# Performance work log

Measured on AMD Instinct MI355X. Metric: run time of the kernel, lower is better.

Reference implementation:

```python
import jax, jax.numpy as jnp
import numpy as np

LN_EPS = 1e-12


def layer_norm(x, g, b):
    mu = jnp.mean(x, axis=-1, keepdims=True)
    var = jnp.mean(jnp.square(x - mu), axis=-1, keepdims=True)
    return (x - mu) * jax.lax.rsqrt(var + LN_EPS) * g + b


def setup_inputs() -> dict:
    key = jax.random.key(0)
    ks = jax.random.split(key, 12)
    B, L, H, P, V = 8, 512, 768, 200, 30522
    src_scores = jax.random.normal(ks[0], (B, L, L), jnp.float32)
    seq_hidden = jax.random.normal(ks[1], (B, L, H), jnp.float32)
    seq_mask = jax.random.randint(ks[2], (B, L), 0, 2).astype(jnp.float32)
    pos_emb = jax.random.normal(ks[3], (512, P), jnp.float32) * 0.02
    Wp = jax.random.normal(ks[4], (H, P), jnp.float32) * 0.02
    bp = jnp.zeros((H,), jnp.float32)
    Wt = jax.random.normal(ks[5], (H, H), jnp.float32) * 0.02
    bt = jnp.zeros((H,), jnp.float32)
    ln_g = jnp.ones((H,), jnp.float32)
    ln_b = jnp.zeros((H,), jnp.float32)
    Wd = jax.random.normal(ks[6], (V, H), jnp.float32) * 0.02
    dec_bias = jnp.zeros((V,), jnp.float32)
    return dict(src_scores=src_scores, seq_hidden=seq_hidden, seq_mask=seq_mask,
                pos_emb=pos_emb, Wp=Wp, bp=bp, Wt=Wt, bt=bt,
                ln_g=ln_g, ln_b=ln_b, Wd=Wd, dec_bias=dec_bias)


def reference(src_scores, seq_hidden, seq_mask, pos_emb, Wp, bp, Wt, bt, ln_g, ln_b, Wd, dec_bias):
    L = src_scores.shape[1]
    # position embeddings for first L positions, projected to hidden size: [L, H]
    pos_h = pos_emb[:L] @ Wp.T + bp
    # pos_scores[b, l, s] = pos_h[l] . seq_hidden[b, s]
    pos_scores = jnp.einsum('lh,bsh->bls', pos_h, seq_hidden)
    scores = pos_scores + src_scores + seq_mask[:, None, :] * -10000.0
    alpha = jax.nn.softmax(scores, axis=-1)                 # [B, L, L]
    seq_sum = jnp.einsum('bls,bsh->blh', alpha, seq_hidden)  # [B, L, H]
    # BertPredictionHeadTransform: dense -> gelu (exact) -> LayerNorm
    h = layer_norm(jax.nn.gelu(seq_sum @ Wt.T + bt, approximate=False), ln_g, ln_b)
    target_scores = h @ Wd.T + dec_bias                      # [B, L, V]
    return target_scores
```

## Files before the change

kernel.cpp:

```cpp
#include <hip/hip_runtime.h>

using f32x4  = __attribute__((ext_vector_type(4))) float;
using short8 = __attribute__((ext_vector_type(8))) short;
using short4v= __attribute__((ext_vector_type(4))) short;
typedef __attribute__((ext_vector_type(8))) __bf16 bf16x8;

__device__ static inline short f2bf(float f){
    unsigned u = __builtin_bit_cast(unsigned, f);
    u += 0x7fffu + ((u >> 16) & 1u);
    return (short)(u >> 16);
}

__device__ static inline void gload_lds16(const void* g, void* l){
    __builtin_amdgcn_global_load_lds(
        (const __attribute__((address_space(1))) void*)g,
        (__attribute__((address_space(3))) void*)l, 16, 0, 0);
}

#define BKK 64

template<int EPI>
__global__ __launch_bounds__(256, 2)
void gemm_bt(const short* __restrict__ A, const short* __restrict__ B,
             float* __restrict__ outF, short* __restrict__ outB,
             const float* __restrict__ bias,
             const float* __restrict__ addmat, const float* __restrict__ mask,
             int K, int ldc, int Ncheck,
             long sA, long sB, long sC, long sX, int maskStride)
{
    __shared__ short Abuf[128*BKK];
    __shared__ short Bbuf[128*BKK];
    const int tid  = threadIdx.x;
    const int wave = tid >> 6;
    const int lane = tid & 63;
    const int bz   = blockIdx.z;
    const int m0   = blockIdx.y * 128;
    const int n0   = blockIdx.x * 128;
    const short* Ab = A + (long)bz * sA;
    const short* Bb = B + (long)bz * sB;

    const int wr = (wave >> 1) * 64;
    const int wc = (wave &  1) * 64;

    f32x4 acc[4][4];
    #pragma unroll
    for (int i=0;i<4;++i)
        #pragma unroll
        for (int j=0;j<4;++j) acc[i][j] = (f32x4){0.f,0.f,0.f,0.f};

    const int srow = wave*32 + (lane >> 3);
    const int kch  = (lane & 7) ^ (lane >> 3);
    const short* gA = Ab + (long)(m0 + srow)*K + kch*8;
    const short* gB = Bb + (long)(n0 + srow)*K + kch*8;
    short* lA = Abuf + wave*32*BKK;
    short* lB = Bbuf + wave*32*BKK;

    for (int k0 = 0; k0 < K; k0 += BKK) {
        __syncthreads();
        #pragma unroll
        for (int is=0; is<4; ++is){
            gload_lds16(gA + k0 + (long)is*8*K, lA + is*8*BKK);
            gload_lds16(gB + k0 + (long)is*8*K, lB + is*8*BKK);
        }
        __syncthreads();
        #pragma unroll
        for (int ks=0; ks<2; ++ks){
            bf16x8 af[4], bfr[4];
            const int chunk = ks*4 + (lane >> 4);
            #pragma unroll
            for (int mi=0;mi<4;++mi){
                int row = wr + mi*16 + (lane & 15);
                af[mi] = *(const bf16x8*)((const char*)Abuf + row*128 + ((chunk ^ (row & 7))<<4));
            }
            #pragma unroll
            for (int ni=0;ni<4;++ni){
                int row = wc + ni*16 + (lane & 15);
                bfr[ni] = *(const bf16x8*)((const char*)Bbuf + row*128 + ((chunk ^ (row & 7))<<4));
            }
            #pragma unroll
            for (int mi=0;mi<4;++mi)
                #pragma unroll
                for (int ni=0;ni<4;++ni)
                    acc[mi][ni] = __builtin_amdgcn_mfma_f32_16x16x32_bf16(af[mi], bfr[ni], acc[mi][ni], 0, 0, 0);
        }
    }

    const int rb = (lane >> 4) * 4;
    const int cb = lane & 15;
    #pragma unroll
    for (int mi=0;mi<4;++mi){
        #pragma unroll
        for (int r=0;r<4;++r){
            const int row = m0 + wr + mi*16 + rb + r;
            #pragma unroll
            for (int ni=0;ni<4;++ni){
                const int col = n0 + wc + ni*16 + cb;
                float v = acc[mi][ni][r];
                if constexpr (EPI == 0) {
                    v += addmat[(long)bz*sX + (long)row*ldc + col]
                         - 10000.f * mask[bz*maskStride + col];
                    outF[(long)bz*sC + (long)row*ldc + col] = v;
                } else if constexpr (EPI == 1) {
                    outB[(long)bz*sC + (long)row*ldc + col] = f2bf(v);
                } else if constexpr (EPI == 3) {
                    if (col < Ncheck) outF[(long)row*ldc + col] = v + bias[col];
                } else if constexpr (EPI == 4) {
                    outB[(long)row*ldc + col] = f2bf(v + bias[col]);
                }
            }
        }
    }
}

__global__ __launch_bounds__(256)
void conv_bf16(const float* __restrict__ in, short* __restrict__ out, long n, long ntot)
{
    const long stride = (long)gridDim.x * 2048;
    for (long i = ((long)blockIdx.x*256 + threadIdx.x)*8; i < ntot; i += stride){
        short8 o = (short8){0,0,0,0,0,0,0,0};
        if (i < n){
            f32x4 a = *(const f32x4*)(in + i);
            f32x4 b = *(const f32x4*)(in + i + 4);
            o[0]=f2bf(a[0]); o[1]=f2bf(a[1]); o[2]=f2bf(a[2]); o[3]=f2bf(a[3]);
            o[4]=f2bf(b[0]); o[5]=f2bf(b[1]); o[6]=f2bf(b[2]); o[7]=f2bf(b[3]);
        }
        *(short8*)(out + i) = o;
    }
}

__global__ __launch_bounds__(256)
void conv_pad(const float* __restrict__ in, short* __restrict__ out,
              int Cin, int Cpad, int total)
{
    int idx = blockIdx.x*256 + threadIdx.x;
    if (idx >= total) return;
    int r = idx / Cpad, c = idx - r*Cpad;
    short v = 0;
    if (c < Cin) v = f2bf(in[(long)r*Cin + c]);
    out[idx] = v;
}

__global__ __launch_bounds__(256)
void transpose_to_bf16(const float* __restrict__ in, short* __restrict__ out, int R, int C)
{
    __shared__ float t[32][33];
    const long boff = (long)blockIdx.z * R * C;
    const float* inb = in + boff;
    short* outb = out + boff;
    int c0 = blockIdx.x*32, r0 = blockIdx.y*32;
    int tx = threadIdx.x & 31, ty = threadIdx.x >> 5;
    #pragma unroll
    for (int j=0;j<32;j+=8) t[ty+j][tx] = inb[(long)(r0+ty+j)*C + c0+tx];
    __syncthreads();
    #pragma unroll
    for (int j=0;j<32;j+=8) outb[(long)(c0+ty+j)*R + r0+tx] = f2bf(t[tx][ty+j]);
}

__global__ __launch_bounds__(256)
void softmax_bf16(const float* __restrict__ scores, short* __restrict__ alpha, int L)
{
    const int row  = blockIdx.x*4 + (threadIdx.x >> 6);
    const int lane = threadIdx.x & 63;
    const float* p = scores + (long)row*L + lane*8;
    f32x4 v0 = *(const f32x4*)p;
    f32x4 v1 = *(const f32x4*)(p+4);
    float x[8] = {v0[0],v0[1],v0[2],v0[3],v1[0],v1[1],v1[2],v1[3]};
    float m = x[0];
    #pragma unroll
    for (int j=1;j<8;++j) m = fmaxf(m, x[j]);
    #pragma unroll
    for (int off=32; off; off>>=1) m = fmaxf(m, __shfl_xor(m, off));
    float s = 0.f;
    #pragma unroll
    for (int j=0;j<8;++j){ x[j] = __expf(x[j]-m); s += x[j]; }
    #pragma unroll
    for (int off=32; off; off>>=1) s += __shfl_xor(s, off);
    const float rinv = 1.f / s;
    short8 o;
    #pragma unroll
    for (int j=0;j<8;++j) o[j] = f2bf(x[j]*rinv);
    *(short8*)(alpha + (long)row*L + lane*8) = o;
}

__global__ __launch_bounds__(256)
void gelu_ln(const float* __restrict__ lin, short* __restrict__ h,
             const float* __restrict__ g, const float* __restrict__ b, int H)
{
    const int row  = blockIdx.x*4 + (threadIdx.x >> 6);
    const int lane = threadIdx.x & 63;
    const float* p = lin + (long)row*H;
    float x[12];
    #pragma unroll
    for (int c=0;c<3;++c){
        f32x4 v = *(const f32x4*)(p + c*256 + lane*4);
        x[c*4+0]=v[0]; x[c*4+1]=v[1]; x[c*4+2]=v[2]; x[c*4+3]=v[3];
    }
    float sum=0.f, sq=0.f;
    #pragma unroll
    for (int j=0;j<12;++j){
        float t = 0.5f * x[j] * (1.f + erff(x[j]*0.70710678118654752f));
        x[j] = t; sum += t; sq += t*t;
    }
    #pragma unroll
    for (int off=32; off; off>>=1){ sum += __shfl_xor(sum, off); sq += __shfl_xor(sq, off); }
    const float mu  = sum * (1.f/768.f);
    const float var = sq  * (1.f/768.f) - mu*mu;
    const float inv = rsqrtf(var + 1e-12f);
    #pragma unroll
    for (int c=0;c<3;++c){
        short4v o;
        #pragma unroll
        for (int j=0;j<4;++j){
            int col = c*256 + lane*4 + j;
            o[j] = f2bf((x[c*4+j]-mu)*inv*g[col] + b[col]);
        }
        *(short4v*)(h + (long)row*H + c*256 + lane*4) = o;
    }
}

extern "C" void kernel_launch(void* const* d_in, const int* in_sizes, int n_in,
                              void* d_out, int out_size, void* d_ws, size_t ws_size,
                              hipStream_t stream)
{
    const float* src_scores = (const float*)d_in[0];
    const float* seq_hidden = (const float*)d_in[1];
    const float* seq_mask   = (const float*)d_in[2];
    const float* pos_emb    = (const float*)d_in[3];
    const float* Wp         = (const float*)d_in[4];
    const float* bp         = (const float*)d_in[5];
    const float* Wt         = (const float*)d_in[6];
    const float* bt         = (const float*)d_in[7];
    const float* ln_g       = (const float*)d_in[8];
    const float* ln_b       = (const float*)d_in[9];
    const float* Wd         = (const float*)d_in[10];
    const float* dec_bias   = (const float*)d_in[11];
    float* out = (float*)d_out;

    const int B=8, L=512, H=768, V=30522, Vp=30592, Kp=256;

    const size_t need = ((size_t)Vp*H + (size_t)B*L*H) * sizeof(short);
    if (ws_size < need) return;
    short* wd_bf = (short*)d_ws;
    short* h_bf  = wd_bf + (long)Vp*H;

    char* sc = (char*)d_out;
    short* sh_nat = (short*)sc;  sc += (long)B*L*H*2;
    short* sh_t   = (short*)sc;  sc += (long)B*L*H*2;
    short* pe_p   = (short*)sc;  sc += (long)L*Kp*2;
    short* wp_p   = (short*)sc;  sc += (long)H*Kp*2;
    short* pos_h  = (short*)sc;  sc += (long)L*H*2;
    short* wt_bf  = (short*)sc;  sc += (long)H*H*2;
    float* scoresb= (float*)sc;  sc += (long)B*L*L*4;
    short* alpha  = (short*)sc;  sc += (long)B*L*L*2;
    short* seqsum = (short*)sc;  sc += (long)B*L*H*2;
    float* lin5   = (float*)sc;  sc += (long)B*L*H*4;

    {   long n=(long)V*H, ntot=(long)Vp*H;
        int blocks=(int)((ntot+2047)/2048); if (blocks>2048) blocks=2048;
        conv_bf16<<<dim3(blocks),256,0,stream>>>(Wd, wd_bf, n, ntot); }
    {   long n=(long)H*H; int blocks=(int)((n+2047)/2048);
        conv_bf16<<<dim3(blocks),256,0,stream>>>(Wt, wt_bf, n, n); }
    {   long n=(long)B*L*H; int blocks=(int)((n+2047)/2048); if (blocks>2048) blocks=2048;
        conv_bf16<<<dim3(blocks),256,0,stream>>>(seq_hidden, sh_nat, n, n); }
    transpose_to_bf16<<<dim3(H/32, L/32, B),256,0,stream>>>(seq_hidden, sh_t, L, H);
    {   int total=L*Kp;
        conv_pad<<<dim3((total+255)/256),256,0,stream>>>(pos_emb, pe_p, 200, Kp, total); }
    {   int total=H*Kp;
        conv_pad<<<dim3((total+255)/256),256,0,stream>>>(Wp, wp_p, 200, Kp, total); }

    gemm_bt<4><<<dim3(H/128, L/128, 1),256,0,stream>>>(
        pe_p, wp_p, nullptr, pos_h, bp, nullptr, nullptr,
        Kp, H, H, 0L, 0L, 0L, 0L, 0);

    gemm_bt<0><<<dim3(L/128, L/128, B),256,0,stream>>>(
        pos_h, sh_nat, scoresb, nullptr, nullptr, src_scores, seq_mask,
        H, L, L, 0L, (long)L*H, (long)L*L, (long)L*L, L);

    softmax_bf16<<<dim3(B*L/4),256,0,stream>>>(scoresb, alpha, L);

    gemm_bt<1><<<dim3(H/128, L/128, B),256,0,stream>>>(
        alpha, sh_t, nullptr, seqsum, nullptr, nullptr, nullptr,
        L, H, H, (long)L*L, (long)H*L, (long)L*H, 0L, 0);

    gemm_bt<3><<<dim3(H/128, (B*L)/128, 1),256,0,stream>>>(
        seqsum, wt_bf, lin5, nullptr, bt, nullptr, nullptr,
        H, H, H, 0L, 0L, 0L, 0L, 0);

    gelu_ln<<<dim3(B*L/4),256,0,stream>>>(lin5, h_bf, ln_g, ln_b, H);

    gemm_bt<3><<<dim3(Vp/128, (B*L)/128, 1),256,0,stream>>>(
        h_bf, wd_bf, out, nullptr, dec_bias, nullptr, nullptr,
        H, V, V, 0L, 0L, 0L, 0L, 0);
}
```

Baseline: 471.1 us.

## Swap GEMM operands for vectorized row stores and add XCD-aware block swizzle

The two large output GEMMs (the transform dense and the vocab decoder) now run with weights as the A operand and activations as B. A new epilogue writes each accumulator's four consecutive output columns as two float2 stores instead of scattered scalar stores. A block-index remap assigns contiguous tiles to each of the eight XCDs to improve L2 reuse of shared operand tiles. In exchange the epilogue adds bounds checks for the ragged vocabulary edge and changes the grid traversal order.

```diff
diff --git a/kernel.cpp b/kernel.cpp
--- a/kernel.cpp
+++ b/kernel.cpp
@@ -1,6 +1,7 @@
 #include <hip/hip_runtime.h>
 
 using f32x4  = __attribute__((ext_vector_type(4))) float;
+using f32x2  = __attribute__((ext_vector_type(2))) float;
 using short8 = __attribute__((ext_vector_type(8))) short;
 using short4v= __attribute__((ext_vector_type(4))) short;
 typedef __attribute__((ext_vector_type(8))) __bf16 bf16x8;
@@ -19,7 +20,7 @@
 
 #define BKK 64
 
-template<int EPI>
+template<int EPI, bool SWZ>
 __global__ __launch_bounds__(256, 2)
 void gemm_bt(const short* __restrict__ A, const short* __restrict__ B,
              float* __restrict__ outF, short* __restrict__ outB,
@@ -34,8 +35,19 @@
     const int wave = tid >> 6;
     const int lane = tid & 63;
     const int bz   = blockIdx.z;
-    const int m0   = blockIdx.y * 128;
-    const int n0   = blockIdx.x * 128;
+
+    int bx = blockIdx.x, by = blockIdx.y;
+    if constexpr (SWZ) {
+        const unsigned GX   = gridDim.x;
+        const unsigned nwg  = GX * gridDim.y;
+        const unsigned orig = blockIdx.y * GX + blockIdx.x;
+        const unsigned q = nwg >> 3, r = nwg & 7;
+        const unsigned xcd = orig & 7, pos = orig >> 3;
+        const unsigned w = (xcd < r ? xcd*(q+1) : r*(q+1) + (xcd-r)*q) + pos;
+        bx = w % GX; by = w / GX;
+    }
+    const int m0 = by * 128;
+    const int n0 = bx * 128;
     const short* Ab = A + (long)bz * sA;
     const short* Bb = B + (long)bz * sB;
 
@@ -87,6 +99,32 @@
 
     const int rb = (lane >> 4) * 4;
     const int cb = lane & 15;
+
+    if constexpr (EPI == 5) {
+        #pragma unroll
+        for (int mi=0;mi<4;++mi){
+            const int v0 = m0 + wr + mi*16 + rb;
+            #pragma unroll
+            for (int ni=0;ni<4;++ni){
+                const int hrow = n0 + wc + ni*16 + cb;
+                float* p = outF + (long)hrow*ldc + v0;
+                if (v0 + 3 < Ncheck) {
+                    f32x2 lo = { acc[mi][ni][0] + bias[v0],
+                                 acc[mi][ni][1] + bias[v0+1] };
+                    f32x2 hi = { acc[mi][ni][2] + bias[v0+2],
+                                 acc[mi][ni][3] + bias[v0+3] };
+                    *(f32x2*)p       = lo;
+                    *(f32x2*)(p + 2) = hi;
+                } else {
+                    #pragma unroll
+                    for (int j=0;j<4;++j)
+                        if (v0 + j < Ncheck) p[j] = acc[mi][ni][j] + bias[v0+j];
+                }
+            }
+        }
+        return;
+    }
+
     #pragma unroll
     for (int mi=0;mi<4;++mi){
         #pragma unroll
@@ -268,27 +306,27 @@
     {   int total=H*Kp;
         conv_pad<<<dim3((total+255)/256),256,0,stream>>>(Wp, wp_p, 200, Kp, total); }
 
-    gemm_bt<4><<<dim3(H/128, L/128, 1),256,0,stream>>>(
+    gemm_bt<4,false><<<dim3(H/128, L/128, 1),256,0,stream>>>(
         pe_p, wp_p, nullptr, pos_h, bp, nullptr, nullptr,
         Kp, H, H, 0L, 0L, 0L, 0L, 0);
 
-    gemm_bt<0><<<dim3(L/128, L/128, B),256,0,stream>>>(
+    gemm_bt<0,false><<<dim3(L/128, L/128, B),256,0,stream>>>(
         pos_h, sh_nat, scoresb, nullptr, nullptr, src_scores, seq_mask,
         H, L, L, 0L, (long)L*H, (long)L*L, (long)L*L, L);
 
     softmax_bf16<<<dim3(B*L/4),256,0,stream>>>(scoresb, alpha, L);
 
-    gemm_bt<1><<<dim3(H/128, L/128, B),256,0,stream>>>(
+    gemm_bt<1,false><<<dim3(H/128, L/128, B),256,0,stream>>>(
         alpha, sh_t, nullptr, seqsum, nullptr, nullptr, nullptr,
         L, H, H, (long)L*L, (long)H*L, (long)L*H, 0L, 0);
 
-    gemm_bt<3><<<dim3(H/128, (B*L)/128, 1),256,0,stream>>>(
-        seqsum, wt_bf, lin5, nullptr, bt, nullptr, nullptr,
+    gemm_bt<5,true><<<dim3((B*L)/128, H/128, 1),256,0,stream>>>(
+        wt_bf, seqsum, lin5, nullptr, bt, nullptr, nullptr,
         H, H, H, 0L, 0L, 0L, 0L, 0);
 
     gelu_ln<<<dim3(B*L/4),256,0,stream>>>(lin5, h_bf, ln_g, ln_b, H);
 
-    gemm_bt<3><<<dim3(Vp/128, (B*L)/128, 1),256,0,stream>>>(
-        h_bf, wd_bf, out, nullptr, dec_bias, nullptr, nullptr,
+    gemm_bt<5,true><<<dim3((B*L)/128, Vp/128, 1),256,0,stream>>>(
+        wd_bf, h_bf, out, nullptr, dec_bias, nullptr, nullptr,
         H, V, V, 0L, 0L, 0L, 0L, 0);
 }
```

Result: slower. 533.6 us (+13.2%).
